# Optimization experiments

Measured on AMD Instinct MI355X. Metric: run time of the kernel, lower is better.

Reference implementation:

```python
import jax, jax.numpy as jnp
import numpy as np

N_NODES = 100000
N_EDGES = 1600000
N_GRAPHS = 1024
HID = 128
NODE_DIM = 7
EDGE_DIM = 3
LAYERS = 4
LN_EPS = 1e-5


def setup_inputs() -> dict:
    key = jax.random.key(0)
    ks = jax.random.split(key, 24)
    s = lambda i, shape, scale=0.05: (jax.random.normal(ks[i], shape, dtype=jnp.float32) * scale)
    x = jax.random.normal(ks[0], (N_NODES, NODE_DIM), dtype=jnp.float32)
    edge_index = jax.random.randint(ks[1], (2, N_EDGES), 0, N_NODES, dtype=jnp.int32)
    edge_attr = jax.random.normal(ks[2], (N_EDGES, EDGE_DIM), dtype=jnp.float32)
    batch = jnp.sort(jax.random.randint(ks[3], (N_NODES,), 0, N_GRAPHS, dtype=jnp.int32))
    return {
        'x': x, 'edge_index': edge_index, 'edge_attr': edge_attr, 'batch': batch,
        'inW': s(4, (NODE_DIM, HID)), 'inb': s(5, (HID,)),
        'edgeW': s(6, (LAYERS, EDGE_DIM, HID)), 'edgeb': s(7, (LAYERS, HID)),
        'w1': s(8, (LAYERS, HID, HID)), 'b1': s(9, (LAYERS, HID)),
        'w2': s(10, (LAYERS, HID, HID)), 'b2': s(11, (LAYERS, HID)),
        'gamma': jnp.ones((LAYERS, HID), dtype=jnp.float32),
        'beta': jnp.zeros((LAYERS, HID), dtype=jnp.float32),
        'fcW1': s(12, (HID, HID)), 'fcb1': s(13, (HID,)),
        'fcW2': s(14, (HID, HID // 2)), 'fcb2': s(15, (HID // 2,)),
        'fcW3': s(16, (HID // 2, 1)), 'fcb3': s(17, (1,)),
    }


def _layernorm(x, gamma, beta):
    mu = jnp.mean(x, axis=-1, keepdims=True)
    var = jnp.mean(jnp.square(x - mu), axis=-1, keepdims=True)
    return (x - mu) * jax.lax.rsqrt(var + LN_EPS) * gamma + beta


def reference(x, edge_index, edge_attr, batch, inW, inb, edgeW, edgeb,
              w1, b1, w2, b2, gamma, beta, fcW1, fcb1, fcW2, fcb2, fcW3, fcb3):
    src, dst = edge_index[0], edge_index[1]
    h = x @ inW + inb  # [N, HID]
    for l in range(LAYERS):
        e = edge_attr @ edgeW[l] + edgeb[l]              # [E, HID]
        msg = jax.nn.relu(h[src] + e)                    # gather + relu
        agg = jax.ops.segment_sum(msg, dst, num_segments=N_NODES)  # scatter-add
        g = agg + h                                      # (1+eps)*x_r with eps=0
        g = jax.nn.relu(g @ w1[l] + b1[l]) @ w2[l] + b2[l]  # GINE MLP
        h = _layernorm(h + jax.nn.relu(g), gamma[l], beta[l])  # residual + LN
    # global mean pool over graphs
    sums = jax.ops.segment_sum(h, batch, num_segments=N_GRAPHS)
    cnt = jax.ops.segment_sum(jnp.ones((h.shape[0],), h.dtype), batch, num_segments=N_GRAPHS)
    pooled = sums / jnp.maximum(cnt, 1.0)[:, None]
    # head (dropout is identity in eval)
    o = jax.nn.relu(pooled @ fcW1 + fcb1)
    o = jax.nn.relu(o @ fcW2 + fcb2)
    return o @ fcW3 + fcb3  # [N_GRAPHS, 1]
```

## Files before the change

kernel.cpp:

```cpp
#include <hip/hip_runtime.h>

#define N_NODES 100000
#define N_EDGES 1600000
#define N_GRAPHS 1024
#define HID 128
#define LAYERS 4
#define LN_EPS 1e-5f
#define NB_SCAN 391
#define GTS 136
#define NB_PROJ 50000
#define NB_WCONV 512
#define NB_EDGE4 1563

typedef __attribute__((ext_vector_type(8))) short bf16x8;
typedef __attribute__((ext_vector_type(4))) float f32x4;

__device__ __forceinline__ unsigned short f2bf(float x) {
    unsigned v = __float_as_uint(x);
    return (unsigned short)((v + 0x7fffu + ((v >> 16) & 1u)) >> 16);
}
__device__ __forceinline__ float bfval(unsigned short u) {
    return __uint_as_float((unsigned)u << 16);
}

__global__ __launch_bounds__(256) void k_prep(
    const float* __restrict__ x, const float* __restrict__ inW,
    const float* __restrict__ inb, float* __restrict__ h,
    unsigned short* __restrict__ hb,
    const float* __restrict__ w1, const float* __restrict__ w2,
    unsigned short* __restrict__ wf_hi, unsigned short* __restrict__ wf_lo) {
    if (blockIdx.x < NB_PROJ) {
        int idx = blockIdx.x * 256 + threadIdx.x;
        int n = idx >> 7, c = idx & 127;
        const float* xr = x + n * 7;
        float s = inb[c];
#pragma unroll
        for (int k = 0; k < 7; ++k) s += xr[k] * inW[k * HID + c];
        h[idx] = s;
        hb[idx] = f2bf(s);
    } else {
        int idx = (blockIdx.x - NB_PROJ) * 256 + threadIdx.x;
        int wid = idx >> 14;
        int layer = wid >> 1, which = wid & 1;
        int within = idx & 16383;
        int nt = within >> 11;
        int ks = (within >> 9) & 3;
        int ln = (within >> 3) & 63;
        int j = within & 7;
        const float* W = (which ? w2 : w1) + layer * HID * HID;
        int k = ks * 32 + (ln >> 4) * 8 + j;
        int n = nt * 16 + (ln & 15);
        float v = W[k * HID + n];
        unsigned short hi = f2bf(v);
        wf_hi[idx] = hi;
        wf_lo[idx] = f2bf(v - bfval(hi));
    }
}

__global__ __launch_bounds__(256) void k_hist(
    const int* __restrict__ ei, int* __restrict__ deg) {
    const int e0 = (blockIdx.x * 256 + threadIdx.x) * 4;
    if (e0 + 4 <= N_EDGES) {
        const int4 d = *(const int4*)(ei + N_EDGES + e0);
        atomicAdd(&deg[d.x], 1);
        atomicAdd(&deg[d.y], 1);
        atomicAdd(&deg[d.z], 1);
        atomicAdd(&deg[d.w], 1);
    }
}

__global__ __launch_bounds__(256) void k_scan1(
    const int* __restrict__ deg, int* __restrict__ bsum) {
    const int i = blockIdx.x * 256 + threadIdx.x;
    int v = (i < N_NODES) ? deg[i] : 0;
#pragma unroll
    for (int off = 1; off < 64; off <<= 1) v += __shfl_xor(v, off);
    __shared__ int wsum[4];
    if ((threadIdx.x & 63) == 0) wsum[threadIdx.x >> 6] = v;
    __syncthreads();
    if (threadIdx.x == 0) bsum[blockIdx.x] = wsum[0] + wsum[1] + wsum[2] + wsum[3];
}

__global__ __launch_bounds__(512) void k_scan2(
    const int* __restrict__ bsum, int* __restrict__ bpre) {
    __shared__ int tmp[512];
    const int t = threadIdx.x;
    int v = (t < NB_SCAN) ? bsum[t] : 0;
    tmp[t] = v;
    __syncthreads();
    for (int off = 1; off < 512; off <<= 1) {
        int u = (t >= off) ? tmp[t - off] : 0;
        __syncthreads();
        tmp[t] += u;
        __syncthreads();
    }
    if (t < NB_SCAN) bpre[t] = tmp[t] - v;
}

__global__ __launch_bounds__(256) void k_scan3(
    const int* __restrict__ deg, const int* __restrict__ bpre,
    int* __restrict__ row_ptr, int* __restrict__ cursor) {
    __shared__ int tmp[256];
    const int t = threadIdx.x;
    const int i = blockIdx.x * 256 + t;
    int d = (i < N_NODES) ? deg[i] : 0;
    tmp[t] = d;
    __syncthreads();
    for (int off = 1; off < 256; off <<= 1) {
        int u = (t >= off) ? tmp[t - off] : 0;
        __syncthreads();
        tmp[t] += u;
        __syncthreads();
    }
    if (i < N_NODES) {
        const int ex = bpre[blockIdx.x] + tmp[t] - d;
        row_ptr[i] = ex;
        cursor[i] = ex;
        if (i == N_NODES - 1) row_ptr[N_NODES] = N_EDGES;
    }
}

__global__ __launch_bounds__(256) void k_scatter(
    const int* __restrict__ ei, const float* __restrict__ ea,
    int* __restrict__ cursor, int* __restrict__ esrc,
    float* __restrict__ eattr) {
    int e = blockIdx.x * 256 + threadIdx.x;
    const int src = ei[e];
    const int dst = ei[N_EDGES + e];
    const float a0 = ea[e * 3 + 0];
    const float a1 = ea[e * 3 + 1];
    const float a2 = ea[e * 3 + 2];
    const int pos = atomicAdd(&cursor[dst], 1);
    esrc[pos] = src;
    eattr[(size_t)pos * 3 + 0] = a0;
    eattr[(size_t)pos * 3 + 1] = a1;
    eattr[(size_t)pos * 3 + 2] = a2;
}

#define FLUSHSTEP {                                                            \
    if (rcur == 0)      { a0x = ax; a0y = ay; rnext = rp2; }                   \
    else if (rcur == 1) { a1x = ax; a1y = ay; rnext = rp3; }                   \
    else                { a2x = ax; a2y = ay; rnext = 0x7fffffff; }            \
    ax = 0.f; ay = 0.f; ++rcur; }

#define EL(JJ)                                                                 \
    const int s##JJ = __builtin_amdgcn_readlane(cS, j + JJ);                   \
    const unsigned gq##JJ = *(const unsigned*)(hbin + (long)s##JJ * HID + c2);

#define EC(JJ) {                                                               \
    const int gi = t + j + (JJ);                                               \
    while (gi >= rnext) FLUSHSTEP                                              \
    const float ax_ = __uint_as_float(__builtin_amdgcn_readlane(__float_as_int(cA0), j + JJ)); \
    const float ay_ = __uint_as_float(__builtin_amdgcn_readlane(__float_as_int(cA1), j + JJ)); \
    const float az_ = __uint_as_float(__builtin_amdgcn_readlane(__float_as_int(cA2), j + JJ)); \
    const float gx = __uint_as_float(gq##JJ << 16) + ebv.x;                    \
    const float gy = __uint_as_float(gq##JJ & 0xffff0000u) + ebv.y;            \
    const float mx = fmaxf(fmaf(az_, ew2.x, fmaf(ay_, ew1.x, fmaf(ax_, ew0.x, gx))), 0.f); \
    const float my = fmaxf(fmaf(az_, ew2.y, fmaf(ay_, ew1.y, fmaf(ax_, ew0.y, gy))), 0.f); \
    ax += mx; ay += my; }

#define ROW_OUT(R, AX, AY) {                                                   \
    const float2 hv = *(const float2*)(h + (long)(nb + (R)) * HID + c2);       \
    const float gx = hv.x + (AX), gy = hv.y + (AY);                            \
    const unsigned short hx = f2bf(gx), hy = f2bf(gy);                         \
    const unsigned short lx = f2bf(gx - bfval(hx)), ly = f2bf(gy - bfval(hy)); \
    *(unsigned*)&gt_hi[(r0 + (R)) * GTS + c2] = (unsigned)hx | ((unsigned)hy << 16); \
    *(unsigned*)&gt_lo[(r0 + (R)) * GTS + c2] = (unsigned)lx | ((unsigned)ly << 16); }

#define T1_OUT(CC, NT) {                                                       \
    const float4 bv = *(const float4*)(b1 + (NT) * 16 + q4);                   \
    const float v0 = fmaxf(CC[0] + bv.x, 0.f);                                 \
    const float v1 = fmaxf(CC[1] + bv.y, 0.f);                                 \
    const float v2 = fmaxf(CC[2] + bv.z, 0.f);                                 \
    const float v3 = fmaxf(CC[3] + bv.w, 0.f);                                 \
    const unsigned short h0_ = f2bf(v0), h1_ = f2bf(v1), h2_ = f2bf(v2), h3_ = f2bf(v3); \
    const unsigned short l0_ = f2bf(v0 - bfval(h0_)), l1_ = f2bf(v1 - bfval(h1_)); \
    const unsigned short l2_ = f2bf(v2 - bfval(h2_)), l3_ = f2bf(v3 - bfval(h3_)); \
    *(uint2*)&t1_hi[ln15 * GTS + (NT) * 16 + q4] =                             \
        make_uint2((unsigned)h0_ | ((unsigned)h1_ << 16), (unsigned)h2_ | ((unsigned)h3_ << 16)); \
    *(uint2*)&t1_lo[ln15 * GTS + (NT) * 16 + q4] =                             \
        make_uint2((unsigned)l0_ | ((unsigned)l1_ << 16), (unsigned)l2_ | ((unsigned)l3_ << 16)); }

__global__ __launch_bounds__(256, 8) void k_node_update(
    const int* __restrict__ esrc, const float* __restrict__ eattr,
    const int* __restrict__ row_ptr,
    const float* __restrict__ eW, const float* __restrict__ eb,
    float* __restrict__ h, const unsigned short* __restrict__ hbin,
    unsigned short* __restrict__ hbout,
    const unsigned short* __restrict__ w1f_hi, const unsigned short* __restrict__ w1f_lo,
    const unsigned short* __restrict__ w2f_hi, const unsigned short* __restrict__ w2f_lo,
    const float* __restrict__ b1, const float* __restrict__ b2,
    const float* __restrict__ gamma, const float* __restrict__ beta) {
    __shared__ __align__(16) unsigned char smem[17408];
    float* stats = (float*)smem;
    unsigned short* gt_hi = (unsigned short*)(smem + 0);
    unsigned short* gt_lo = (unsigned short*)(smem + 4352);
    unsigned short* t1_hi = (unsigned short*)(smem + 8704);
    unsigned short* t1_lo = (unsigned short*)(smem + 13056);

    const int wave = threadIdx.x >> 6;
    const int lane = threadIdx.x & 63;
    const int n0 = blockIdx.x * 16;
    const int r0 = wave * 4;
    const int c2 = lane * 2;

    {
        const float2 ew0 = *(const float2*)(eW + 0 * HID + c2);
        const float2 ew1 = *(const float2*)(eW + 1 * HID + c2);
        const float2 ew2 = *(const float2*)(eW + 2 * HID + c2);
        const float2 ebv = *(const float2*)(eb + c2);
        const int nb = n0 + r0;
        const int rp0 = __builtin_amdgcn_readfirstlane(row_ptr[nb + 0]);
        const int rp1 = __builtin_amdgcn_readfirstlane(row_ptr[nb + 1]);
        const int rp2 = __builtin_amdgcn_readfirstlane(row_ptr[nb + 2]);
        const int rp3 = __builtin_amdgcn_readfirstlane(row_ptr[nb + 3]);
        const int rp4 = __builtin_amdgcn_readfirstlane(row_ptr[nb + 4]);

        float a0x = 0.f, a0y = 0.f, a1x = 0.f, a1y = 0.f;
        float a2x = 0.f, a2y = 0.f, a3x = 0.f, a3y = 0.f;
        float ax = 0.f, ay = 0.f;
        int rcur = 0;
        int rnext = rp1;

        int cS, nS;
        float cA0, cA1, cA2, nA0, nA1, nA2;
        if (rp0 + lane < rp4) {
            cS = esrc[rp0 + lane];
            cA0 = eattr[(size_t)(rp0 + lane) * 3 + 0];
            cA1 = eattr[(size_t)(rp0 + lane) * 3 + 1];
            cA2 = eattr[(size_t)(rp0 + lane) * 3 + 2];
        }
        for (int t = rp0; t < rp4; t += 64) {
            const int cnt = (rp4 - t < 64) ? (rp4 - t) : 64;
            if (t + 64 + lane < rp4) {
                nS = esrc[t + 64 + lane];
                nA0 = eattr[(size_t)(t + 64 + lane) * 3 + 0];
                nA1 = eattr[(size_t)(t + 64 + lane) * 3 + 1];
                nA2 = eattr[(size_t)(t + 64 + lane) * 3 + 2];
            }
            int j = 0;
            for (; j + 16 <= cnt; j += 16) {
                EL(0) EL(1) EL(2) EL(3) EL(4) EL(5) EL(6) EL(7)
                EL(8) EL(9) EL(10) EL(11) EL(12) EL(13) EL(14) EL(15)
                EC(0) EC(1) EC(2) EC(3) EC(4) EC(5) EC(6) EC(7)
                EC(8) EC(9) EC(10) EC(11) EC(12) EC(13) EC(14) EC(15)
            }
            for (; j + 4 <= cnt; j += 4) {
                EL(0) EL(1) EL(2) EL(3)
                EC(0) EC(1) EC(2) EC(3)
            }
            for (; j < cnt; ++j) {
                EL(0)
                EC(0)
            }
            cS = nS; cA0 = nA0; cA1 = nA1; cA2 = nA2;
        }
        if (rcur == 0)      { a0x = ax; a0y = ay; }
        else if (rcur == 1) { a1x = ax; a1y = ay; }
        else if (rcur == 2) { a2x = ax; a2y = ay; }
        else                { a3x = ax; a3y = ay; }
        ROW_OUT(0, a0x, a0y)
        ROW_OUT(1, a1x, a1y)
        ROW_OUT(2, a2x, a2y)
        ROW_OUT(3, a3x, a3y)
    }
    __syncthreads();

    const int ln15 = lane & 15;
    const int q8 = (lane >> 4) * 8;
    const int q4 = (lane >> 4) * 4;
    const int nt0 = wave * 2, nt1 = nt0 + 1;

    {
        f32x4 c0 = {0.f, 0.f, 0.f, 0.f};
        f32x4 c1 = {0.f, 0.f, 0.f, 0.f};
#pragma unroll
        for (int ks = 0; ks < 4; ++ks) {
            const bf16x8 bh = *(const bf16x8*)&gt_hi[ln15 * GTS + ks * 32 + q8];
            const bf16x8 bl = *(const bf16x8*)&gt_lo[ln15 * GTS + ks * 32 + q8];
            const bf16x8 a0h = *(const bf16x8*)(w1f_hi + (((nt0 * 4 + ks) * 64 + lane) << 3));
            const bf16x8 a0l = *(const bf16x8*)(w1f_lo + (((nt0 * 4 + ks) * 64 + lane) << 3));
            const bf16x8 a1h = *(const bf16x8*)(w1f_hi + (((nt1 * 4 + ks) * 64 + lane) << 3));
            const bf16x8 a1l = *(const bf16x8*)(w1f_lo + (((nt1 * 4 + ks) * 64 + lane) << 3));
            c0 = __builtin_amdgcn_mfma_f32_16x16x32_bf16(a0h, bh, c0, 0, 0, 0);
            c0 = __builtin_amdgcn_mfma_f32_16x16x32_bf16(a0h, bl, c0, 0, 0, 0);
            c0 = __builtin_amdgcn_mfma_f32_16x16x32_bf16(a0l, bh, c0, 0, 0, 0);
            c1 = __builtin_amdgcn_mfma_f32_16x16x32_bf16(a1h, bh, c1, 0, 0, 0);
            c1 = __builtin_amdgcn_mfma_f32_16x16x32_bf16(a1h, bl, c1, 0, 0, 0);
            c1 = __builtin_amdgcn_mfma_f32_16x16x32_bf16(a1l, bh, c1, 0, 0, 0);
        }
        T1_OUT(c0, nt0)
        T1_OUT(c1, nt1)
    }
    __syncthreads();

    {
        f32x4 c0 = {0.f, 0.f, 0.f, 0.f};
        f32x4 c1 = {0.f, 0.f, 0.f, 0.f};
#pragma unroll
        for (int ks = 0; ks < 4; ++ks) {
            const bf16x8 bh = *(const bf16x8*)&t1_hi[ln15 * GTS + ks * 32 + q8];
            const bf16x8 bl = *(const bf16x8*)&t1_lo[ln15 * GTS + ks * 32 + q8];
            const bf16x8 a0h = *(const bf16x8*)(w2f_hi + (((nt0 * 4 + ks) * 64 + lane) << 3));
            const bf16x8 a0l = *(const bf16x8*)(w2f_lo + (((nt0 * 4 + ks) * 64 + lane) << 3));
            const bf16x8 a1h = *(const bf16x8*)(w2f_hi + (((nt1 * 4 + ks) * 64 + lane) << 3));
            const bf16x8 a1l = *(const bf16x8*)(w2f_lo + (((nt1 * 4 + ks) * 64 + lane) << 3));
            c0 = __builtin_amdgcn_mfma_f32_16x16x32_bf16(a0h, bh, c0, 0, 0, 0);
            c0 = __builtin_amdgcn_mfma_f32_16x16x32_bf16(a0h, bl, c0, 0, 0, 0);
            c0 = __builtin_amdgcn_mfma_f32_16x16x32_bf16(a0l, bh, c0, 0, 0, 0);
            c1 = __builtin_amdgcn_mfma_f32_16x16x32_bf16(a1h, bh, c1, 0, 0, 0);
            c1 = __builtin_amdgcn_mfma_f32_16x16x32_bf16(a1h, bl, c1, 0, 0, 0);
            c1 = __builtin_amdgcn_mfma_f32_16x16x32_bf16(a1l, bh, c1, 0, 0, 0);
        }
        const int row = n0 + ln15;
        const float4 b20 = *(const float4*)(b2 + nt0 * 16 + q4);
        const float4 b21 = *(const float4*)(b2 + nt1 * 16 + q4);
        const float4 hv0 = *(const float4*)(h + (long)row * HID + nt0 * 16 + q4);
        const float4 hv1 = *(const float4*)(h + (long)row * HID + nt1 * 16 + q4);
        float4 u0, u1;
        u0.x = hv0.x + fmaxf(c0[0] + b20.x, 0.f);
        u0.y = hv0.y + fmaxf(c0[1] + b20.y, 0.f);
        u0.z = hv0.z + fmaxf(c0[2] + b20.z, 0.f);
        u0.w = hv0.w + fmaxf(c0[3] + b20.w, 0.f);
        u1.x = hv1.x + fmaxf(c1[0] + b21.x, 0.f);
        u1.y = hv1.y + fmaxf(c1[1] + b21.y, 0.f);
        u1.z = hv1.z + fmaxf(c1[2] + b21.z, 0.f);
        u1.w = hv1.w + fmaxf(c1[3] + b21.w, 0.f);
        float s = u0.x + u0.y + u0.z + u0.w + u1.x + u1.y + u1.z + u1.w;
        float s2 = u0.x * u0.x + u0.y * u0.y + u0.z * u0.z + u0.w * u0.w +
                   u1.x * u1.x + u1.y * u1.y + u1.z * u1.z + u1.w * u1.w;
        s += __shfl_xor(s, 16); s2 += __shfl_xor(s2, 16);
        s += __shfl_xor(s, 32); s2 += __shfl_xor(s2, 32);
        if (lane < 16) {
            stats[wave * 32 + lane * 2 + 0] = s;
            stats[wave * 32 + lane * 2 + 1] = s2;
        }
        __syncthreads();
        const float S  = stats[0 * 32 + ln15 * 2] + stats[1 * 32 + ln15 * 2] +
                         stats[2 * 32 + ln15 * 2] + stats[3 * 32 + ln15 * 2];
        const float S2 = stats[0 * 32 + ln15 * 2 + 1] + stats[1 * 32 + ln15 * 2 + 1] +
                         stats[2 * 32 + ln15 * 2 + 1] + stats[3 * 32 + ln15 * 2 + 1];
        const float mu = S * (1.f / HID);
        const float var = S2 * (1.f / HID) - mu * mu;
        const float inv = rsqrtf(var + LN_EPS);
        const float4 gm0 = *(const float4*)(gamma + nt0 * 16 + q4);
        const float4 gm1 = *(const float4*)(gamma + nt1 * 16 + q4);
        const float4 bt0 = *(const float4*)(beta + nt0 * 16 + q4);
        const float4 bt1 = *(const float4*)(beta + nt1 * 16 + q4);
        float4 o0, o1;
        o0.x = (u0.x - mu) * inv * gm0.x + bt0.x;
        o0.y = (u0.y - mu) * inv * gm0.y + bt0.y;
        o0.z = (u0.z - mu) * inv * gm0.z + bt0.z;
        o0.w = (u0.w - mu) * inv * gm0.w + bt0.w;
        o1.x = (u1.x - mu) * inv * gm1.x + bt1.x;
        o1.y = (u1.y - mu) * inv * gm1.y + bt1.y;
        o1.z = (u1.z - mu) * inv * gm1.z + bt1.z;
        o1.w = (u1.w - mu) * inv * gm1.w + bt1.w;
        *(float4*)(h + (long)row * HID + nt0 * 16 + q4) = o0;
        *(float4*)(h + (long)row * HID + nt1 * 16 + q4) = o1;
        *(uint2*)(hbout + (long)row * HID + nt0 * 16 + q4) =
            make_uint2((unsigned)f2bf(o0.x) | ((unsigned)f2bf(o0.y) << 16),
                       (unsigned)f2bf(o0.z) | ((unsigned)f2bf(o0.w) << 16));
        *(uint2*)(hbout + (long)row * HID + nt1 * 16 + q4) =
            make_uint2((unsigned)f2bf(o1.x) | ((unsigned)f2bf(o1.y) << 16),
                       (unsigned)f2bf(o1.z) | ((unsigned)f2bf(o1.w) << 16));
    }
}

__global__ __launch_bounds__(128) void k_pool(
    const float* __restrict__ h, const int* __restrict__ batch,
    float* __restrict__ sums, float* __restrict__ cnt) {
    const int c = threadIdx.x;
    const int n0 = blockIdx.x * 64;
    if (n0 >= N_NODES) return;
    const int nend = min(n0 + 64, N_NODES);
    int cur = batch[n0];
    float acc = 0.f;
    int runlen = 0;
    for (int n = n0; n < nend; ++n) {
        const int b = batch[n];
        if (b != cur) {
            atomicAdd(&sums[(long)cur * HID + c], acc);
            if (c == 0) atomicAdd(&cnt[cur], (float)runlen);
            acc = 0.f;
            runlen = 0;
            cur = b;
        }
        acc += h[(long)n * HID + c];
        ++runlen;
    }
    atomicAdd(&sums[(long)cur * HID + c], acc);
    if (c == 0) atomicAdd(&cnt[cur], (float)runlen);
}

__global__ __launch_bounds__(128) void k_head(
    const float* __restrict__ sums, const float* __restrict__ cnt,
    const float* __restrict__ fcW1, const float* __restrict__ fcb1,
    const float* __restrict__ fcW2, const float* __restrict__ fcb2,
    const float* __restrict__ fcW3, const float* __restrict__ fcb3,
    float* __restrict__ out) {
    __shared__ float p[HID];
    __shared__ float o1[HID];
    __shared__ float o2[64];
    const int g = blockIdx.x, t = threadIdx.x;
    const float c = fmaxf(cnt[g], 1.0f);
    p[t] = sums[g * HID + t] / c;
    __syncthreads();
    float s = fcb1[t];
    for (int k = 0; k < HID; ++k) s += p[k] * fcW1[k * HID + t];
    o1[t] = fmaxf(s, 0.f);
    __syncthreads();
    if (t < 64) {
        float s2 = fcb2[t];
        for (int k = 0; k < HID; ++k) s2 += o1[k] * fcW2[k * 64 + t];
        o2[t] = fmaxf(s2, 0.f);
    }
    __syncthreads();
    if (t < 64) {
        float v = o2[t] * fcW3[t];
#pragma unroll
        for (int off = 32; off > 0; off >>= 1) v += __shfl_down(v, off);
        if (t == 0) out[g] = v + fcb3[0];
    }
}

extern "C" void kernel_launch(void* const* d_in, const int* in_sizes, int n_in,
                              void* d_out, int out_size, void* d_ws, size_t ws_size,
                              hipStream_t stream) {
    const float* x    = (const float*)d_in[0];
    const int*   ei   = (const int*)d_in[1];
    const float* ea   = (const float*)d_in[2];
    const int*   batch= (const int*)d_in[3];
    const float* inW  = (const float*)d_in[4];
    const float* inb  = (const float*)d_in[5];
    const float* edgeW= (const float*)d_in[6];
    const float* edgeb= (const float*)d_in[7];
    const float* w1   = (const float*)d_in[8];
    const float* b1   = (const float*)d_in[9];
    const float* w2   = (const float*)d_in[10];
    const float* b2   = (const float*)d_in[11];
    const float* gamma= (const float*)d_in[12];
    const float* beta = (const float*)d_in[13];
    const float* fcW1 = (const float*)d_in[14];
    const float* fcb1 = (const float*)d_in[15];
    const float* fcW2 = (const float*)d_in[16];
    const float* fcb2 = (const float*)d_in[17];
    const float* fcW3 = (const float*)d_in[18];
    const float* fcb3 = (const float*)d_in[19];
    float* out = (float*)d_out;

    float* eattr = (float*)d_ws;
    float* h     = eattr + (size_t)N_EDGES * 3;
    unsigned short* hb0 = (unsigned short*)(h + (size_t)N_NODES * HID);
    unsigned short* hb1 = hb0 + (size_t)N_NODES * HID;
    unsigned short* wf_hi = hb1 + (size_t)N_NODES * HID;
    unsigned short* wf_lo = wf_hi + LAYERS * 2 * 16384;
    int*    esrc    = (int*)(wf_lo + LAYERS * 2 * 16384);
    int*    row_ptr = esrc + N_EDGES;
    int*    cursor  = row_ptr + (N_NODES + 1);
    int*    deg     = cursor + N_NODES;
    int*    bsum    = deg + N_NODES;
    int*    bpre    = bsum + 512;
    float*  sums    = (float*)(bpre + 512);
    float*  cnt     = sums + (size_t)N_GRAPHS * HID;
    const size_t zbytes = (N_NODES + 512 + 512) * sizeof(int) +
                          ((size_t)N_GRAPHS * HID + N_GRAPHS) * sizeof(float);

    hipMemsetAsync(deg, 0, zbytes, stream);

    k_prep<<<NB_PROJ + NB_WCONV, 256, 0, stream>>>(x, inW, inb, h, hb0,
                                                   w1, w2, wf_hi, wf_lo);

    k_hist<<<NB_EDGE4, 256, 0, stream>>>(ei, deg);
    k_scan1<<<NB_SCAN, 256, 0, stream>>>(deg, bsum);
    k_scan2<<<1, 512, 0, stream>>>(bsum, bpre);
    k_scan3<<<NB_SCAN, 256, 0, stream>>>(deg, bpre, row_ptr, cursor);
    k_scatter<<<N_EDGES / 256, 256, 0, stream>>>(ei, ea, cursor, esrc, eattr);

    unsigned short* hbin = hb0;
    unsigned short* hbout = hb1;
    for (int l = 0; l < LAYERS; ++l) {
        k_node_update<<<N_NODES / 16, 256, 0, stream>>>(
            esrc, eattr, row_ptr, edgeW + l * 3 * HID, edgeb + l * HID,
            h, hbin, hbout,
            wf_hi + (l * 2 + 0) * 16384, wf_lo + (l * 2 + 0) * 16384,
            wf_hi + (l * 2 + 1) * 16384, wf_lo + (l * 2 + 1) * 16384,
            b1 + l * HID, b2 + l * HID, gamma + l * HID, beta + l * HID);
        unsigned short* tmp = hbin; hbin = hbout; hbout = tmp;
    }

    k_pool<<<(N_NODES + 63) / 64, 128, 0, stream>>>(h, batch, sums, cnt);
    k_head<<<N_GRAPHS, 128, 0, stream>>>(sums, cnt, fcW1, fcb1, fcW2, fcb2,
                                         fcW3, fcb3, out);
}
```

Measured before the change: 737.9 us.

## Replace per-node atomic edge scatter with two-pass bucketed sort into CSR

Edges are first scattered into 64-node buckets as packed 16-byte records, using one atomic per edge on a bucket cursor. A second kernel then sorts each bucket in shared memory and writes the source indices and edge attributes contiguously. The aim is to replace scattered small writes with coalesced ones, at the cost of an extra pass and a temporary buffer that reuses the hb1 activation buffer.

```diff
diff --git a/kernel.cpp b/kernel.cpp
--- a/kernel.cpp
+++ b/kernel.cpp
@@ -11,6 +11,8 @@
 #define NB_PROJ 50000
 #define NB_WCONV 512
 #define NB_EDGE4 1563
+#define NBUCK 1563
+#define BCAP 2048
 
 typedef __attribute__((ext_vector_type(8))) short bf16x8;
 typedef __attribute__((ext_vector_type(4))) float f32x4;
@@ -99,7 +101,7 @@
 
 __global__ __launch_bounds__(256) void k_scan3(
     const int* __restrict__ deg, const int* __restrict__ bpre,
-    int* __restrict__ row_ptr, int* __restrict__ cursor) {
+    int* __restrict__ row_ptr, int* __restrict__ bcur) {
     __shared__ int tmp[256];
     const int t = threadIdx.x;
     const int i = blockIdx.x * 256 + t;
@@ -115,26 +117,71 @@
     if (i < N_NODES) {
         const int ex = bpre[blockIdx.x] + tmp[t] - d;
         row_ptr[i] = ex;
-        cursor[i] = ex;
+        if ((i & 63) == 0) bcur[i >> 6] = ex;
         if (i == N_NODES - 1) row_ptr[N_NODES] = N_EDGES;
     }
 }
 
-__global__ __launch_bounds__(256) void k_scatter(
+__global__ __launch_bounds__(256) void k_binscat(
     const int* __restrict__ ei, const float* __restrict__ ea,
-    int* __restrict__ cursor, int* __restrict__ esrc,
-    float* __restrict__ eattr) {
-    int e = blockIdx.x * 256 + threadIdx.x;
+    int* __restrict__ bcur, int4* __restrict__ erec) {
+    const int e = blockIdx.x * 256 + threadIdx.x;
     const int src = ei[e];
     const int dst = ei[N_EDGES + e];
     const float a0 = ea[e * 3 + 0];
     const float a1 = ea[e * 3 + 1];
     const float a2 = ea[e * 3 + 2];
-    const int pos = atomicAdd(&cursor[dst], 1);
-    esrc[pos] = src;
-    eattr[(size_t)pos * 3 + 0] = a0;
-    eattr[(size_t)pos * 3 + 1] = a1;
-    eattr[(size_t)pos * 3 + 2] = a2;
+    const int pos = atomicAdd(&bcur[dst >> 6], 1);
+    int4 r;
+    r.x = src | ((dst & 63) << 20);
+    r.y = __float_as_int(a0);
+    r.z = __float_as_int(a1);
+    r.w = __float_as_int(a2);
+    erec[pos] = r;
+}
+
+__global__ __launch_bounds__(256) void k_bucketsort(
+    const int4* __restrict__ erec, const int* __restrict__ row_ptr,
+    int* __restrict__ esrc, float* __restrict__ eattr) {
+    __shared__ int lcur[64];
+    __shared__ int4 stage[BCAP];
+    const int b = blockIdx.x;
+    const int nb0 = b << 6;
+    const int nb1 = (nb0 + 64 < N_NODES) ? nb0 + 64 : N_NODES;
+    const int base = row_ptr[nb0];
+    const int end = row_ptr[nb1];
+    const int cnt = end - base;
+    if (threadIdx.x < 64) {
+        const int node = nb0 + threadIdx.x;
+        lcur[threadIdx.x] = ((node < nb1) ? row_ptr[node] : end) - base;
+    }
+    __syncthreads();
+    if (cnt <= BCAP) {
+        for (int i = threadIdx.x; i < cnt; i += 256) {
+            const int4 r = erec[base + i];
+            const int row = (r.x >> 20) & 63;
+            const int pos = atomicAdd(&lcur[row], 1);
+            stage[pos] = r;
+        }
+        __syncthreads();
+        for (int i = threadIdx.x; i < cnt; i += 256)
+            esrc[base + i] = stage[i].x & 0xFFFFF;
+        float* ef = eattr + (size_t)base * 3;
+        const float* sf = (const float*)stage;
+        const int m = cnt * 3;
+        for (int t = threadIdx.x; t < m; t += 256)
+            ef[t] = sf[(t / 3) * 4 + 1 + (t % 3)];
+    } else {
+        for (int i = threadIdx.x; i < cnt; i += 256) {
+            const int4 r = erec[base + i];
+            const int row = (r.x >> 20) & 63;
+            const int pos = base + atomicAdd(&lcur[row], 1);
+            esrc[pos] = r.x & 0xFFFFF;
+            eattr[(size_t)pos * 3 + 0] = __int_as_float(r.y);
+            eattr[(size_t)pos * 3 + 1] = __int_as_float(r.z);
+            eattr[(size_t)pos * 3 + 2] = __int_as_float(r.w);
+        }
+    }
 }
 
 #define FLUSHSTEP {                                                            \
@@ -457,14 +504,15 @@
     unsigned short* wf_lo = wf_hi + LAYERS * 2 * 16384;
     int*    esrc    = (int*)(wf_lo + LAYERS * 2 * 16384);
     int*    row_ptr = esrc + N_EDGES;
-    int*    cursor  = row_ptr + (N_NODES + 1);
-    int*    deg     = cursor + N_NODES;
+    int*    bcur    = row_ptr + (N_NODES + 1);
+    int*    deg     = bcur + N_NODES;
     int*    bsum    = deg + N_NODES;
     int*    bpre    = bsum + 512;
     float*  sums    = (float*)(bpre + 512);
     float*  cnt     = sums + (size_t)N_GRAPHS * HID;
     const size_t zbytes = (N_NODES + 512 + 512) * sizeof(int) +
                           ((size_t)N_GRAPHS * HID + N_GRAPHS) * sizeof(float);
+    int4*   erec    = (int4*)hb1;
 
     hipMemsetAsync(deg, 0, zbytes, stream);
 
@@ -474,8 +522,9 @@
     k_hist<<<NB_EDGE4, 256, 0, stream>>>(ei, deg);
     k_scan1<<<NB_SCAN, 256, 0, stream>>>(deg, bsum);
     k_scan2<<<1, 512, 0, stream>>>(bsum, bpre);
-    k_scan3<<<NB_SCAN, 256, 0, stream>>>(deg, bpre, row_ptr, cursor);
-    k_scatter<<<N_EDGES / 256, 256, 0, stream>>>(ei, ea, cursor, esrc, eattr);
+    k_scan3<<<NB_SCAN, 256, 0, stream>>>(deg, bpre, row_ptr, bcur);
+    k_binscat<<<N_EDGES / 256, 256, 0, stream>>>(ei, ea, bcur, erec);
+    k_bucketsort<<<NBUCK, 256, 0, stream>>>(erec, row_ptr, esrc, eattr);
 
     unsigned short* hbin = hb0;
     unsigned short* hbout = hb1;
```

New measurement: 891.8 us. +20.8%, slower.
